# Optimization experiments

Measured on AMD Instinct MI355X. Metric: run time of the kernel, lower is better.

## Reference

```python
import jax, jax.numpy as jnp
import numpy as np

NUM_USERS = 100000
NUM_ITEMS = 50000
N = NUM_USERS + NUM_ITEMS
EMB = 64
N_LAYERS = 3
N_EDGES = 4800000
BATCH = 4096


def setup_inputs() -> dict:
    key = jax.random.key(0)
    ks = jax.random.split(key, 8)
    users = jax.random.randint(ks[0], (BATCH,), 0, NUM_USERS, dtype=jnp.int64 if jax.config.jax_enable_x64 else jnp.int32)
    pos_items = jax.random.randint(ks[1], (BATCH,), 0, NUM_ITEMS)
    neg_items = jax.random.randint(ks[2], (BATCH,), 0, NUM_ITEMS)
    adj_rows = jax.random.randint(ks[3], (N_EDGES,), 0, N)
    adj_cols = jax.random.randint(ks[4], (N_EDGES,), 0, N)
    # scale values like a degree-normalized adjacency (~1/deg) to keep magnitudes stable
    adj_vals = jax.random.uniform(ks[5], (N_EDGES,), dtype=jnp.float32) * (1.0 / 32.0)
    user_emb = jax.random.normal(ks[6], (NUM_USERS, EMB), dtype=jnp.float32) * 0.1
    item_emb = jax.random.normal(ks[7], (NUM_ITEMS, EMB), dtype=jnp.float32) * 0.1
    return {"users": users, "pos_items": pos_items, "neg_items": neg_items,
            "adj_rows": adj_rows, "adj_cols": adj_cols, "adj_vals": adj_vals,
            "user_emb": user_emb, "item_emb": item_emb}


def _spmm(rows, cols, vals, x):
    # sparse (N,N) @ dense (N,E): gather columns, scale, scatter-add to rows
    gathered = x[cols] * vals[:, None]          # [n_edges, EMB]
    return jax.ops.segment_sum(gathered, rows, num_segments=N)


def reference(users, pos_items, neg_items, adj_rows, adj_cols, adj_vals, user_emb, item_emb):
    emb = jnp.concatenate([user_emb, item_emb], axis=0)  # [N, EMB]
    acc = emb
    cur = emb
    for _ in range(N_LAYERS):
        cur = _spmm(adj_rows, adj_cols, adj_vals, cur)
        acc = acc + cur
    final = acc / (N_LAYERS + 1)                # layer-wise mean
    users_emb = final[:NUM_USERS]
    items_emb = final[NUM_USERS:]
    u = users_emb[users]                        # [B, EMB]
    pos = items_emb[pos_items]
    neg = items_emb[neg_items]
    pos_scores = jnp.sum(u * pos, axis=1)       # [B]
    neg_scores = jnp.sum(u * neg, axis=1)
    return (pos_scores, neg_scores)
```

## Files before the change

kernel.cpp:

```cpp
#include <hip/hip_runtime.h>

#define NUM_USERS 100000
#define NUM_ITEMS 50000
#define NNODES    150000
#define EMB       64
#define NEDGES    4800000
#define BATCH     4096
#define BUCKETS   293
#define BROWS     512
#define EPB       8192
#define NBLK_A    586
#define CAP       17408
#define NSAMP     (3 * BATCH)

typedef unsigned short u16;
typedef unsigned int   u32;

__device__ inline float bf2f(u16 u) { return __uint_as_float(((u32)u) << 16); }
__device__ inline u16 f2bf(float f) {
    u32 b = __float_as_uint(f);
    b += 0x7FFFu + ((b >> 16) & 1u);
    return (u16)(b >> 16);
}
__device__ inline u32 pack2(float a, float b) {
    return (u32)f2bf(a) | ((u32)f2bf(b) << 16);
}

__global__ void init_kernel(const float* __restrict__ user_emb,
                            const float* __restrict__ item_emb,
                            u16* __restrict__ l0) {
    long i = (long)blockIdx.x * blockDim.x + threadIdx.x;
    const long n4 = (long)NNODES * EMB / 4;
    if (i >= n4) return;
    const long nu4 = (long)NUM_USERS * EMB / 4;
    float4 v = (i < nu4) ? ((const float4*)user_emb)[i]
                         : ((const float4*)item_emb)[i - nu4];
    ushort4 o;
    o.x = f2bf(v.x); o.y = f2bf(v.y); o.z = f2bf(v.z); o.w = f2bf(v.w);
    ((ushort4*)l0)[i] = o;
}

__global__ void __launch_bounds__(512) binA_kernel(const int* __restrict__ rows,
                                                   const int* __restrict__ cols,
                                                   const float* __restrict__ vals,
                                                   int* __restrict__ bfill,
                                                   int2* __restrict__ tmp) {
    __shared__ int2 ebuf[EPB];
    __shared__ int  hist[BUCKETS];
    __shared__ int  start[BUCKETS];
    __shared__ int  cursor[BUCKETS];
    __shared__ int  gbase[BUCKETS];
    const int tid = threadIdx.x;
    for (int i = tid; i < BUCKETS; i += 512) hist[i] = 0;
    __syncthreads();

    const long base = (long)blockIdx.x * EPB;
    int rsave[16];
    #pragma unroll
    for (int k = 0; k < 16; ++k) {
        long e = base + (long)k * 512 + tid;
        int r = -1;
        if (e < NEDGES) {
            r = rows[e];
            atomicAdd(&hist[r >> 9], 1);
        }
        rsave[k] = r;
    }
    __syncthreads();

    if (tid < 64) {
        int carry = 0;
        for (int cb = 0; cb < BUCKETS; cb += 64) {
            int i = cb + tid;
            int orig = (i < BUCKETS) ? hist[i] : 0;
            int x = orig;
            #pragma unroll
            for (int d = 1; d < 64; d <<= 1) {
                int t = __shfl_up(x, d, 64);
                if (tid >= d) x += t;
            }
            int total = __shfl(x, 63, 64);
            if (i < BUCKETS) { start[i] = x - orig + carry; cursor[i] = x - orig + carry; }
            carry += total;
        }
    }
    __syncthreads();

    for (int b = tid; b < BUCKETS; b += 512) {
        int h = hist[b];
        gbase[b] = h ? b * CAP + atomicAdd(&bfill[b], h) : 0;
    }

    #pragma unroll
    for (int k = 0; k < 16; ++k) {
        int r = rsave[k];
        if (r >= 0) {
            long e = base + (long)k * 512 + tid;
            int pos = atomicAdd(&cursor[r >> 9], 1);
            ebuf[pos] = make_int2(((r & 511) << 18) | cols[e], __float_as_int(vals[e]));
        }
    }
    __syncthreads();

    const int wv = tid >> 6, lane = tid & 63;
    const int* eb32 = (const int*)ebuf;
    int* gtmp = (int*)tmp;
    for (int b = wv; b < BUCKETS; b += 8) {
        int cnt2 = hist[b] * 2;
        if (!cnt2) continue;
        int  s2 = start[b] * 2;
        long d2 = (long)gbase[b] * 2;
        for (int i = lane; i < cnt2; i += 64)
            gtmp[d2 + i] = eb32[s2 + i];
    }
}

__global__ void scan_buckets(const int* __restrict__ bfill, int* __restrict__ bucketBase) {
    int lane = threadIdx.x;
    int carry = 0;
    for (int cb = 0; cb < BUCKETS; cb += 64) {
        int i = cb + lane;
        int orig = (i < BUCKETS) ? bfill[i] : 0;
        int x = orig;
        #pragma unroll
        for (int d = 1; d < 64; d <<= 1) {
            int t = __shfl_up(x, d, 64);
            if (lane >= d) x += t;
        }
        int total = __shfl(x, 63, 64);
        if (i < BUCKETS) bucketBase[i] = x - orig + carry;
        carry += total;
    }
}

__global__ void __launch_bounds__(512) binB_kernel(const int* __restrict__ bfill,
                                                   const int* __restrict__ bucketBase,
                                                   const int2* __restrict__ tmp,
                                                   int* __restrict__ rowPtr,
                                                   int2* __restrict__ csr) {
    const int bucket = blockIdx.x;
    __shared__ int lhist[BROWS];
    __shared__ int rp[BROWS];
    __shared__ int fill[BROWS];
    const int t = threadIdx.x;
    lhist[t] = 0; fill[t] = 0;
    __syncthreads();

    const int cnt = bfill[bucket];
    const int2* src = tmp + (long)bucket * CAP;
    for (int k = t; k < cnt; k += 512)
        atomicAdd(&lhist[src[k].x >> 18], 1);
    __syncthreads();

    const int gb = bucketBase[bucket];
    if (t < 64) {
        int carry = 0;
        for (int cb = 0; cb < BROWS; cb += 64) {
            int i = cb + t;
            int orig = lhist[i];
            int x = orig;
            #pragma unroll
            for (int d = 1; d < 64; d <<= 1) {
                int tt = __shfl_up(x, d, 64);
                if (t >= d) x += tt;
            }
            int total = __shfl(x, 63, 64);
            rp[i] = x - orig + carry + gb;
            carry += total;
        }
    }
    __syncthreads();

    int rowIdx = bucket * BROWS + t;
    rowPtr[rowIdx] = rp[t];

    for (int k = t; k < cnt; k += 512) {
        int2 p = src[k];
        int rL = p.x >> 18;
        int pos = rp[rL] + atomicAdd(&fill[rL], 1);
        csr[pos] = make_int2(p.x & 0x3FFFF, p.y);
    }
}

#define ACCX(V, X) { \
    a[0] += (V) * __uint_as_float((X).x << 16); \
    a[1] += (V) * __uint_as_float((X).x & 0xFFFF0000u); \
    a[2] += (V) * __uint_as_float((X).y << 16); \
    a[3] += (V) * __uint_as_float((X).y & 0xFFFF0000u); \
    a[4] += (V) * __uint_as_float((X).z << 16); \
    a[5] += (V) * __uint_as_float((X).z & 0xFFFF0000u); \
    a[6] += (V) * __uint_as_float((X).w << 16); \
    a[7] += (V) * __uint_as_float((X).w & 0xFFFF0000u); }

__global__ void spmm_csr(const int* __restrict__ rowPtr, const int2* __restrict__ csr,
                         const u16* __restrict__ cur, u16* __restrict__ nxt) {
    int gtid = blockIdx.x * blockDim.x + threadIdx.x;
    int row = gtid >> 3;
    int t   = gtid & 7;
    if (row >= NNODES) return;
    int beg = rowPtr[row], end = rowPtr[row + 1];
    float a[8];
    #pragma unroll
    for (int i = 0; i < 8; ++i) a[i] = 0.f;

    int e = beg;
    for (; e + 7 < end; e += 8) {
        int2 p[8];
        #pragma unroll
        for (int j = 0; j < 8; ++j) p[j] = csr[e + j];
        uint4 x[8];
        #pragma unroll
        for (int j = 0; j < 8; ++j)
            x[j] = *(const uint4*)(cur + ((long)p[j].x << 6) + (t << 3));
        #pragma unroll
        for (int j = 0; j < 8; ++j) {
            float v = __int_as_float(p[j].y);
            ACCX(v, x[j]);
        }
    }
    for (; e < end; ++e) {
        int2 p = csr[e];
        float v = __int_as_float(p.y);
        uint4 x = *(const uint4*)(cur + ((long)p.x << 6) + (t << 3));
        ACCX(v, x);
    }

    uint4 o;
    o.x = pack2(a[0], a[1]);
    o.y = pack2(a[2], a[3]);
    o.z = pack2(a[4], a[5]);
    o.w = pack2(a[6], a[7]);
    *(uint4*)(nxt + ((long)row << 6) + (t << 3)) = o;
}

__global__ void spmm_sampled(const int* __restrict__ users,
                             const int* __restrict__ pos_items,
                             const int* __restrict__ neg_items,
                             const int* __restrict__ rowPtr, const int2* __restrict__ csr,
                             const u16* __restrict__ cur, float* __restrict__ sampled) {
    int gtid = blockIdx.x * blockDim.x + threadIdx.x;
    int slot = gtid >> 3;
    int t    = gtid & 7;
    if (slot >= NSAMP) return;
    int row;
    if (slot < BATCH)          row = users[slot];
    else if (slot < 2 * BATCH) row = pos_items[slot - BATCH] + NUM_USERS;
    else                       row = neg_items[slot - 2 * BATCH] + NUM_USERS;

    int beg = rowPtr[row], end = rowPtr[row + 1];
    float a[8];
    #pragma unroll
    for (int i = 0; i < 8; ++i) a[i] = 0.f;

    int e = beg;
    for (; e + 7 < end; e += 8) {
        int2 p[8];
        #pragma unroll
        for (int j = 0; j < 8; ++j) p[j] = csr[e + j];
        uint4 x[8];
        #pragma unroll
        for (int j = 0; j < 8; ++j)
            x[j] = *(const uint4*)(cur + ((long)p[j].x << 6) + (t << 3));
        #pragma unroll
        for (int j = 0; j < 8; ++j) {
            float v = __int_as_float(p[j].y);
            ACCX(v, x[j]);
        }
    }
    for (; e < end; ++e) {
        int2 p = csr[e];
        float v = __int_as_float(p.y);
        uint4 x = *(const uint4*)(cur + ((long)p.x << 6) + (t << 3));
        ACCX(v, x);
    }

    float4* dst = (float4*)(sampled + ((long)slot << 6) + (t << 3));
    dst[0] = make_float4(a[0], a[1], a[2], a[3]);
    dst[1] = make_float4(a[4], a[5], a[6], a[7]);
}

__global__ void score_kernel(const int* __restrict__ users,
                             const int* __restrict__ pos_items,
                             const int* __restrict__ neg_items,
                             const float* __restrict__ uemb,
                             const float* __restrict__ iemb,
                             const u16* __restrict__ l1,
                             const u16* __restrict__ l2,
                             const float* __restrict__ sampled,
                             float* __restrict__ out) {
    int gtid = blockIdx.x * blockDim.x + threadIdx.x;
    int wave = gtid >> 6;
    int lane = threadIdx.x & 63;
    if (wave >= BATCH) return;
    int u = users[wave];
    int p = pos_items[wave];
    int n = neg_items[wave];
    long U = (long)u * EMB + lane;
    long P = (long)(p + NUM_USERS) * EMB + lane;
    long N = (long)(n + NUM_USERS) * EMB + lane;
    float ue = uemb[(long)u * EMB + lane] + bf2f(l1[U]) + bf2f(l2[U])
             + sampled[(long)wave * EMB + lane];
    float pe = iemb[(long)p * EMB + lane] + bf2f(l1[P]) + bf2f(l2[P])
             + sampled[(long)(BATCH + wave) * EMB + lane];
    float ne = iemb[(long)n * EMB + lane] + bf2f(l1[N]) + bf2f(l2[N])
             + sampled[(long)(2 * BATCH + wave) * EMB + lane];
    float ps = ue * pe;
    float ns = ue * ne;
    #pragma unroll
    for (int off = 32; off > 0; off >>= 1) {
        ps += __shfl_down(ps, off, 64);
        ns += __shfl_down(ns, off, 64);
    }
    if (lane == 0) {
        out[wave]         = ps * 0.0625f;
        out[BATCH + wave] = ns * 0.0625f;
    }
}

extern "C" void kernel_launch(void* const* d_in, const int* in_sizes, int n_in,
                              void* d_out, int out_size, void* d_ws, size_t ws_size,
                              hipStream_t stream) {
    const int*   users = (const int*)d_in[0];
    const int*   pos   = (const int*)d_in[1];
    const int*   neg   = (const int*)d_in[2];
    const int*   rows  = (const int*)d_in[3];
    const int*   cols  = (const int*)d_in[4];
    const float* vals  = (const float*)d_in[5];
    const float* uemb  = (const float*)d_in[6];
    const float* iemb  = (const float*)d_in[7];
    float* out = (float*)d_out;

    const size_t tblElems = (size_t)NNODES * EMB;
    u16*  B0      = (u16*)d_ws;
    u16*  B1      = B0 + tblElems;
    u16*  B2      = B1 + tblElems;
    int2* tmp     = (int2*)(B2 + tblElems);
    int2* csr     = (int2*)(tmp + (size_t)BUCKETS * CAP);
    int*  rowPtr  = (int*)(csr + NEDGES);
    int*  bfill   = rowPtr + 150016;
    int*  bucketB = bfill + 320;
    float* sampled= (float*)(bucketB + 320);

    hipMemsetAsync(bfill, 0, 320 * sizeof(int), stream);

    binA_kernel<<<NBLK_A, 512, 0, stream>>>(rows, cols, vals, bfill, tmp);
    scan_buckets<<<1, 64, 0, stream>>>(bfill, bucketB);
    binB_kernel<<<BUCKETS, 512, 0, stream>>>(bfill, bucketB, tmp, rowPtr, csr);

    const long n4 = (long)tblElems / 4;
    init_kernel<<<(int)((n4 + 255) / 256), 256, 0, stream>>>(uemb, iemb, B0);

    const long nth = (long)NNODES * 8;
    const int  spmmGrid = (int)((nth + 255) / 256);
    spmm_csr<<<spmmGrid, 256, 0, stream>>>(rowPtr, csr, B0, B1);
    spmm_csr<<<spmmGrid, 256, 0, stream>>>(rowPtr, csr, B1, B2);
    spmm_sampled<<<(NSAMP * 8 + 255) / 256, 256, 0, stream>>>(users, pos, neg,
                                                              rowPtr, csr, B2, sampled);

    score_kernel<<<(BATCH * 64) / 256, 256, 0, stream>>>(users, pos, neg,
                                                         uemb, iemb, B1, B2, sampled, out);
}
```

Before: 456.3 us.

## Replace two-pass bucketed COO-to-CSR binning with global histogram, scan, atomic scatter

Replaces the two-stage, shared-memory bucketed sort (binA/binB through a temp buffer) with a direct CSR build. A per-row global atomic histogram feeds a chunked exclusive scan (chunk scan, partials scan, add-back), and a scatter kernel then places each edge using an atomic per-row fill counter. This drops the intermediate temp buffer and its extra read/write pass, and adds nontemporal loads. In exchange it relies on many scattered global atomics and random csr writes, and edge order within a row becomes nondeterministic.

```diff
diff --git a/kernel.cpp b/kernel.cpp
--- a/kernel.cpp
+++ b/kernel.cpp
@@ -6,15 +6,15 @@
 #define EMB       64
 #define NEDGES    4800000
 #define BATCH     4096
-#define BUCKETS   293
-#define BROWS     512
-#define EPB       8192
-#define NBLK_A    586
-#define CAP       17408
 #define NSAMP     (3 * BATCH)
+#define RP_ALLOC  150528
+#define NCHUNK    147
 
 typedef unsigned short u16;
 typedef unsigned int   u32;
+typedef unsigned long long u64;
+typedef float f32x4 __attribute__((ext_vector_type(4)));
+typedef int   i32x4 __attribute__((ext_vector_type(4)));
 
 __device__ inline float bf2f(u16 u) { return __uint_as_float(((u32)u) << 16); }
 __device__ inline u16 f2bf(float f) {
@@ -33,94 +33,63 @@
     const long n4 = (long)NNODES * EMB / 4;
     if (i >= n4) return;
     const long nu4 = (long)NUM_USERS * EMB / 4;
-    float4 v = (i < nu4) ? ((const float4*)user_emb)[i]
-                         : ((const float4*)item_emb)[i - nu4];
+    f32x4 v;
+    if (i < nu4) v = __builtin_nontemporal_load((const f32x4*)user_emb + i);
+    else         v = __builtin_nontemporal_load((const f32x4*)item_emb + (i - nu4));
     ushort4 o;
     o.x = f2bf(v.x); o.y = f2bf(v.y); o.z = f2bf(v.z); o.w = f2bf(v.w);
     ((ushort4*)l0)[i] = o;
 }
 
-__global__ void __launch_bounds__(512) binA_kernel(const int* __restrict__ rows,
-                                                   const int* __restrict__ cols,
-                                                   const float* __restrict__ vals,
-                                                   int* __restrict__ bfill,
-                                                   int2* __restrict__ tmp) {
-    __shared__ int2 ebuf[EPB];
-    __shared__ int  hist[BUCKETS];
-    __shared__ int  start[BUCKETS];
-    __shared__ int  cursor[BUCKETS];
-    __shared__ int  gbase[BUCKETS];
+
+__global__ void hist_kernel(const int* __restrict__ rows, int* __restrict__ cnt) {
+    long i = (long)blockIdx.x * blockDim.x + threadIdx.x;
+    if (i >= NEDGES / 4) return;
+    i32x4 r = __builtin_nontemporal_load((const i32x4*)rows + i);
+    atomicAdd(&cnt[r.x], 1);
+    atomicAdd(&cnt[r.y], 1);
+    atomicAdd(&cnt[r.z], 1);
+    atomicAdd(&cnt[r.w], 1);
+}
+
+__global__ void __launch_bounds__(1024) chunkscan_kernel(const int* __restrict__ cnt,
+                                                         int* __restrict__ rowPtr,
+                                                         int* __restrict__ partials) {
+    __shared__ int wsum[16];
+    const int b   = blockIdx.x;
     const int tid = threadIdx.x;
-    for (int i = tid; i < BUCKETS; i += 512) hist[i] = 0;
+    const int wid = tid >> 6, lane = tid & 63;
+    const int i = b * 1024 + tid;
+    int v = (i < NNODES + 1) ? cnt[i] : 0;
+    int x = v;
+    #pragma unroll
+    for (int d = 1; d < 64; d <<= 1) {
+        int t = __shfl_up(x, d, 64);
+        if (lane >= d) x += t;
+    }
+    if (lane == 63) wsum[wid] = x;
     __syncthreads();
-
-    const long base = (long)blockIdx.x * EPB;
-    int rsave[16];
-    #pragma unroll
-    for (int k = 0; k < 16; ++k) {
-        long e = base + (long)k * 512 + tid;
-        int r = -1;
-        if (e < NEDGES) {
-            r = rows[e];
-            atomicAdd(&hist[r >> 9], 1);
+    if (tid < 16) {
+        int s = wsum[tid];
+        #pragma unroll
+        for (int d = 1; d < 16; d <<= 1) {
+            int t = __shfl_up(s, d, 16);
+            if (tid >= d) s += t;
         }
-        rsave[k] = r;
+        wsum[tid] = s;
     }
     __syncthreads();
-
-    if (tid < 64) {
-        int carry = 0;
-        for (int cb = 0; cb < BUCKETS; cb += 64) {
-            int i = cb + tid;
-            int orig = (i < BUCKETS) ? hist[i] : 0;
-            int x = orig;
-            #pragma unroll
-            for (int d = 1; d < 64; d <<= 1) {
-                int t = __shfl_up(x, d, 64);
-                if (tid >= d) x += t;
-            }
-            int total = __shfl(x, 63, 64);
-            if (i < BUCKETS) { start[i] = x - orig + carry; cursor[i] = x - orig + carry; }
-            carry += total;
-        }
-    }
-    __syncthreads();
-
-    for (int b = tid; b < BUCKETS; b += 512) {
-        int h = hist[b];
-        gbase[b] = h ? b * CAP + atomicAdd(&bfill[b], h) : 0;
-    }
-
-    #pragma unroll
-    for (int k = 0; k < 16; ++k) {
-        int r = rsave[k];
-        if (r >= 0) {
-            long e = base + (long)k * 512 + tid;
-            int pos = atomicAdd(&cursor[r >> 9], 1);
-            ebuf[pos] = make_int2(((r & 511) << 18) | cols[e], __float_as_int(vals[e]));
-        }
-    }
-    __syncthreads();
-
-    const int wv = tid >> 6, lane = tid & 63;
-    const int* eb32 = (const int*)ebuf;
-    int* gtmp = (int*)tmp;
-    for (int b = wv; b < BUCKETS; b += 8) {
-        int cnt2 = hist[b] * 2;
-        if (!cnt2) continue;
-        int  s2 = start[b] * 2;
-        long d2 = (long)gbase[b] * 2;
-        for (int i = lane; i < cnt2; i += 64)
-            gtmp[d2 + i] = eb32[s2 + i];
-    }
-}
-
-__global__ void scan_buckets(const int* __restrict__ bfill, int* __restrict__ bucketBase) {
+    int woff = wid ? wsum[wid - 1] : 0;
+    rowPtr[i] = x - v + woff;
+    if (tid == 0) partials[b] = wsum[15];
+}
+
+__global__ void scanpart_kernel(int* __restrict__ partials) {
     int lane = threadIdx.x;
     int carry = 0;
-    for (int cb = 0; cb < BUCKETS; cb += 64) {
+    for (int cb = 0; cb < NCHUNK; cb += 64) {
         int i = cb + lane;
-        int orig = (i < BUCKETS) ? bfill[i] : 0;
+        int orig = (i < NCHUNK) ? partials[i] : 0;
         int x = orig;
         #pragma unroll
         for (int d = 1; d < 64; d <<= 1) {
@@ -128,58 +97,29 @@
             if (lane >= d) x += t;
         }
         int total = __shfl(x, 63, 64);
-        if (i < BUCKETS) bucketBase[i] = x - orig + carry;
+        if (i < NCHUNK) partials[i] = x - orig + carry;
         carry += total;
     }
 }
 
-__global__ void __launch_bounds__(512) binB_kernel(const int* __restrict__ bfill,
-                                                   const int* __restrict__ bucketBase,
-                                                   const int2* __restrict__ tmp,
-                                                   int* __restrict__ rowPtr,
-                                                   int2* __restrict__ csr) {
-    const int bucket = blockIdx.x;
-    __shared__ int lhist[BROWS];
-    __shared__ int rp[BROWS];
-    __shared__ int fill[BROWS];
-    const int t = threadIdx.x;
-    lhist[t] = 0; fill[t] = 0;
-    __syncthreads();
-
-    const int cnt = bfill[bucket];
-    const int2* src = tmp + (long)bucket * CAP;
-    for (int k = t; k < cnt; k += 512)
-        atomicAdd(&lhist[src[k].x >> 18], 1);
-    __syncthreads();
-
-    const int gb = bucketBase[bucket];
-    if (t < 64) {
-        int carry = 0;
-        for (int cb = 0; cb < BROWS; cb += 64) {
-            int i = cb + t;
-            int orig = lhist[i];
-            int x = orig;
-            #pragma unroll
-            for (int d = 1; d < 64; d <<= 1) {
-                int tt = __shfl_up(x, d, 64);
-                if (t >= d) x += tt;
-            }
-            int total = __shfl(x, 63, 64);
-            rp[i] = x - orig + carry + gb;
-            carry += total;
-        }
-    }
-    __syncthreads();
-
-    int rowIdx = bucket * BROWS + t;
-    rowPtr[rowIdx] = rp[t];
-
-    for (int k = t; k < cnt; k += 512) {
-        int2 p = src[k];
-        int rL = p.x >> 18;
-        int pos = rp[rL] + atomicAdd(&fill[rL], 1);
-        csr[pos] = make_int2(p.x & 0x3FFFF, p.y);
-    }
+__global__ void __launch_bounds__(1024) addback_kernel(int* __restrict__ rowPtr,
+                                                       const int* __restrict__ partials) {
+    rowPtr[blockIdx.x * 1024 + threadIdx.x] += partials[blockIdx.x];
+}
+
+__global__ void scatter_kernel(const int* __restrict__ rows,
+                               const int* __restrict__ cols,
+                               const float* __restrict__ vals,
+                               const int* __restrict__ rowPtr,
+                               int* __restrict__ fill,
+                               int2* __restrict__ csr) {
+    long e = (long)blockIdx.x * blockDim.x + threadIdx.x;
+    if (e >= NEDGES) return;
+    int r = __builtin_nontemporal_load(rows + e);
+    int c = __builtin_nontemporal_load(cols + e);
+    float v = __builtin_nontemporal_load(vals + e);
+    int pos = rowPtr[r] + atomicAdd(&fill[r], 1);
+    csr[pos] = make_int2(c, __float_as_int(v));
 }
 
 #define ACCX(V, X) { \
@@ -334,21 +274,24 @@
     u16*  B0      = (u16*)d_ws;
     u16*  B1      = B0 + tblElems;
     u16*  B2      = B1 + tblElems;
-    int2* tmp     = (int2*)(B2 + tblElems);
-    int2* csr     = (int2*)(tmp + (size_t)BUCKETS * CAP);
+    int2* csr     = (int2*)(B2 + tblElems);
     int*  rowPtr  = (int*)(csr + NEDGES);
-    int*  bfill   = rowPtr + 150016;
-    int*  bucketB = bfill + 320;
-    float* sampled= (float*)(bucketB + 320);
-
-    hipMemsetAsync(bfill, 0, 320 * sizeof(int), stream);
-
-    binA_kernel<<<NBLK_A, 512, 0, stream>>>(rows, cols, vals, bfill, tmp);
-    scan_buckets<<<1, 64, 0, stream>>>(bfill, bucketB);
-    binB_kernel<<<BUCKETS, 512, 0, stream>>>(bfill, bucketB, tmp, rowPtr, csr);
+    int*  cnt     = rowPtr + RP_ALLOC;
+    int*  fill    = cnt + RP_ALLOC;
+    int*  partials= fill + RP_ALLOC;
+    float* sampled= (float*)(partials + 256);
+
+    (void)hipMemsetAsync(cnt, 0, (size_t)2 * RP_ALLOC * sizeof(int), stream);
 
     const long n4 = (long)tblElems / 4;
     init_kernel<<<(int)((n4 + 255) / 256), 256, 0, stream>>>(uemb, iemb, B0);
+
+    hist_kernel<<<(NEDGES / 4 + 255) / 256, 256, 0, stream>>>(rows, cnt);
+    chunkscan_kernel<<<NCHUNK, 1024, 0, stream>>>(cnt, rowPtr, partials);
+    scanpart_kernel<<<1, 64, 0, stream>>>(partials);
+    addback_kernel<<<NCHUNK, 1024, 0, stream>>>(rowPtr, partials);
+    scatter_kernel<<<(NEDGES + 255) / 256, 256, 0, stream>>>(rows, cols, vals,
+                                                             rowPtr, fill, csr);
 
     const long nth = (long)NNODES * 8;
     const int  spmmGrid = (int)((nth + 255) / 256);
```

New measurement: 790.9 us. 73.3% more time.

## Enlarge binning blocks, fold bucket scan into binB, use nontemporal loads

Applied to the files above, without the earlier changes.

Each binA block now handles 15360 edges in 30 rounds, so the grid is roughly halved. The separate scan_buckets launch is removed and each binB block computes its own global base with a wave reduction over bfill. Edge and embedding input reads use nontemporal loads, and the bucket copy-out moves 8-byte elements instead of 4-byte ones. init_kernel is launched before binning. The larger per-block LDS buffer and longer register array may lower occupancy, and the prefix-sum work inside binB is repeated per bucket.

```diff
diff --git a/kernel.cpp b/kernel.cpp
--- a/kernel.cpp
+++ b/kernel.cpp
@@ -8,13 +8,16 @@
 #define BATCH     4096
 #define BUCKETS   293
 #define BROWS     512
-#define EPB       8192
-#define NBLK_A    586
+#define EPB       15360
+#define NROUND    30
+#define NBLK_A    313
 #define CAP       17408
 #define NSAMP     (3 * BATCH)
 
 typedef unsigned short u16;
 typedef unsigned int   u32;
+typedef unsigned long long u64;
+typedef float f32x4 __attribute__((ext_vector_type(4)));
 
 __device__ inline float bf2f(u16 u) { return __uint_as_float(((u32)u) << 16); }
 __device__ inline u16 f2bf(float f) {
@@ -33,8 +36,9 @@
     const long n4 = (long)NNODES * EMB / 4;
     if (i >= n4) return;
     const long nu4 = (long)NUM_USERS * EMB / 4;
-    float4 v = (i < nu4) ? ((const float4*)user_emb)[i]
-                         : ((const float4*)item_emb)[i - nu4];
+    f32x4 v;
+    if (i < nu4) v = __builtin_nontemporal_load((const f32x4*)user_emb + i);
+    else         v = __builtin_nontemporal_load((const f32x4*)item_emb + (i - nu4));
     ushort4 o;
     o.x = f2bf(v.x); o.y = f2bf(v.y); o.z = f2bf(v.z); o.w = f2bf(v.w);
     ((ushort4*)l0)[i] = o;
@@ -55,13 +59,13 @@
     __syncthreads();
 
     const long base = (long)blockIdx.x * EPB;
-    int rsave[16];
-    #pragma unroll
-    for (int k = 0; k < 16; ++k) {
+    int rsave[NROUND];
+    #pragma unroll
+    for (int k = 0; k < NROUND; ++k) {
         long e = base + (long)k * 512 + tid;
         int r = -1;
         if (e < NEDGES) {
-            r = rows[e];
+            r = __builtin_nontemporal_load(rows + e);
             atomicAdd(&hist[r >> 9], 1);
         }
         rsave[k] = r;
@@ -92,49 +96,32 @@
     }
 
     #pragma unroll
-    for (int k = 0; k < 16; ++k) {
+    for (int k = 0; k < NROUND; ++k) {
         int r = rsave[k];
         if (r >= 0) {
             long e = base + (long)k * 512 + tid;
             int pos = atomicAdd(&cursor[r >> 9], 1);
-            ebuf[pos] = make_int2(((r & 511) << 18) | cols[e], __float_as_int(vals[e]));
+            int c = __builtin_nontemporal_load(cols + e);
+            float v = __builtin_nontemporal_load(vals + e);
+            ebuf[pos] = make_int2(((r & 511) << 18) | c, __float_as_int(v));
         }
     }
     __syncthreads();
 
     const int wv = tid >> 6, lane = tid & 63;
-    const int* eb32 = (const int*)ebuf;
-    int* gtmp = (int*)tmp;
+    const u64* eb8 = (const u64*)ebuf;
+    u64* gt8 = (u64*)tmp;
     for (int b = wv; b < BUCKETS; b += 8) {
-        int cnt2 = hist[b] * 2;
-        if (!cnt2) continue;
-        int  s2 = start[b] * 2;
-        long d2 = (long)gbase[b] * 2;
-        for (int i = lane; i < cnt2; i += 64)
-            gtmp[d2 + i] = eb32[s2 + i];
-    }
-}
-
-__global__ void scan_buckets(const int* __restrict__ bfill, int* __restrict__ bucketBase) {
-    int lane = threadIdx.x;
-    int carry = 0;
-    for (int cb = 0; cb < BUCKETS; cb += 64) {
-        int i = cb + lane;
-        int orig = (i < BUCKETS) ? bfill[i] : 0;
-        int x = orig;
-        #pragma unroll
-        for (int d = 1; d < 64; d <<= 1) {
-            int t = __shfl_up(x, d, 64);
-            if (lane >= d) x += t;
-        }
-        int total = __shfl(x, 63, 64);
-        if (i < BUCKETS) bucketBase[i] = x - orig + carry;
-        carry += total;
+        int cnt = hist[b];
+        if (!cnt) continue;
+        int  s = start[b];
+        long d = (long)gbase[b];
+        for (int i = lane; i < cnt; i += 64)
+            gt8[d + i] = eb8[s + i];
     }
 }
 
 __global__ void __launch_bounds__(512) binB_kernel(const int* __restrict__ bfill,
-                                                   const int* __restrict__ bucketBase,
                                                    const int2* __restrict__ tmp,
                                                    int* __restrict__ rowPtr,
                                                    int2* __restrict__ csr) {
@@ -152,8 +139,13 @@
         atomicAdd(&lhist[src[k].x >> 18], 1);
     __syncthreads();
 
-    const int gb = bucketBase[bucket];
     if (t < 64) {
+        int s = 0;
+        for (int i = t; i < bucket; i += 64) s += bfill[i];
+        #pragma unroll
+        for (int off = 32; off > 0; off >>= 1) s += __shfl_down(s, off, 64);
+        int gb = __shfl(s, 0, 64);
+
         int carry = 0;
         for (int cb = 0; cb < BROWS; cb += 64) {
             int i = cb + t;
@@ -338,17 +330,15 @@
     int2* csr     = (int2*)(tmp + (size_t)BUCKETS * CAP);
     int*  rowPtr  = (int*)(csr + NEDGES);
     int*  bfill   = rowPtr + 150016;
-    int*  bucketB = bfill + 320;
-    float* sampled= (float*)(bucketB + 320);
-
-    hipMemsetAsync(bfill, 0, 320 * sizeof(int), stream);
-
-    binA_kernel<<<NBLK_A, 512, 0, stream>>>(rows, cols, vals, bfill, tmp);
-    scan_buckets<<<1, 64, 0, stream>>>(bfill, bucketB);
-    binB_kernel<<<BUCKETS, 512, 0, stream>>>(bfill, bucketB, tmp, rowPtr, csr);
+    float* sampled= (float*)(bfill + 320);
+
+    (void)hipMemsetAsync(bfill, 0, 320 * sizeof(int), stream);
 
     const long n4 = (long)tblElems / 4;
     init_kernel<<<(int)((n4 + 255) / 256), 256, 0, stream>>>(uemb, iemb, B0);
+
+    binA_kernel<<<NBLK_A, 512, 0, stream>>>(rows, cols, vals, bfill, tmp);
+    binB_kernel<<<BUCKETS, 512, 0, stream>>>(bfill, tmp, rowPtr, csr);
 
     const long nth = (long)NNODES * 8;
     const int  spmmGrid = (int)((nth + 255) / 256);
```

New measurement: 456.3 us. No clear change (-0.0%).
